# Kernel optimization log

Hardware: AMD Instinct MI355X
Metric: run time of the kernel (lower is better)

The kernel has to match this reference:

```python
import jax, jax.numpy as jnp
import numpy as np

N, T, F = 4096, 24, 16          # nodes, seq_len, in_features
H = 128                          # temporal_hidden
NH, DO = 4, 32                   # gat num_heads, gat out_features (NH*DO == H)
SEM, PH = 64, 32                 # semantic hidden, predictor hidden
SLOPE = 0.2                      # leaky_relu negative slope
ADJ_P = 0.01                     # adjacency density


def setup_inputs() -> dict:
    key = jax.random.key(0)
    ks = jax.random.split(key, 40)
    f32 = jnp.float32

    def rn(k, shape, s=0.02):
        return jax.random.normal(k, shape, f32) * s

    features = jax.random.normal(ks[0], (N, T, F), f32)
    pos_adj = (jax.random.uniform(ks[1], (N, N)) < ADJ_P).astype(f32)
    neg_adj = (jax.random.uniform(ks[2], (N, N)) < ADJ_P).astype(f32)

    inp = dict(features=features, pos_adj=pos_adj, neg_adj=neg_adj)
    # GRU (torch layout: W_ih [3H,F], W_hh [3H,H], gate order r,z,n)
    inp['gru_Wih'] = rn(ks[3], (3 * H, F), 1.0 / np.sqrt(H))
    inp['gru_Whh'] = rn(ks[4], (3 * H, H), 1.0 / np.sqrt(H))
    inp['gru_bih'] = rn(ks[5], (3 * H,), 1.0 / np.sqrt(H))
    inp['gru_bhh'] = rn(ks[6], (3 * H,), 1.0 / np.sqrt(H))
    # GAT params (linear weights stored [in, out] so we use x @ W)
    i = 7
    for pre in ('pos', 'neg'):
        inp[pre + '_W'] = rn(ks[i], (H, NH * DO)); i += 1
        inp[pre + '_u'] = rn(ks[i], (NH, DO, 1), 1.0); i += 1
        inp[pre + '_v'] = rn(ks[i], (NH, DO, 1), 1.0); i += 1
        inp[pre + '_b'] = rn(ks[i], (1, NH * DO)); i += 1
        inp[pre + '_pW'] = rn(ks[i], (H, NH * DO)); i += 1
        inp[pre + '_pb'] = jnp.zeros((NH * DO,), f32)
    inp['self_W'] = rn(ks[i], (H, H)); i += 1
    inp['self_b'] = jnp.zeros((H,), f32)
    inp['mpos_W'] = rn(ks[i], (NH * DO, H)); i += 1
    inp['mpos_b'] = jnp.zeros((H,), f32)
    inp['mneg_W'] = rn(ks[i], (NH * DO, H)); i += 1
    inp['mneg_b'] = jnp.zeros((H,), f32)
    inp['sem_W1'] = rn(ks[i], (H, SEM)); i += 1
    inp['sem_b1'] = jnp.zeros((SEM,), f32)
    inp['sem_W2'] = rn(ks[i], (SEM, 1)); i += 1
    inp['pred_W1'] = rn(ks[i], (H, PH)); i += 1
    inp['pred_b1'] = jnp.zeros((PH,), f32)
    inp['pred_W2'] = rn(ks[i], (PH, 1)); i += 1
    inp['pred_b2'] = jnp.zeros((1,), f32)
    return inp


def _gru_last(x, Wih, Whh, bih, bhh):
    # x: [N, T, F] -> last hidden state [N, H]
    gi_all = jnp.einsum('ntf,gf->tng', x, Wih) + bih  # precompute input gates [T,N,3H]
    h0 = jnp.zeros((x.shape[0], Whh.shape[1]), x.dtype)

    def step(h, gi):
        gh = h @ Whh.T + bhh
        ir, iz, in_ = jnp.split(gi, 3, axis=-1)
        hr, hz, hn = jnp.split(gh, 3, axis=-1)
        r = jax.nn.sigmoid(ir + hr)
        z = jax.nn.sigmoid(iz + hz)
        n = jnp.tanh(in_ + r * hn)
        return (1.0 - z) * n + z * h, None

    h, _ = jax.lax.scan(step, h0, gi_all)
    return h


def _gat(x, adj, W, u, v, b, pW, pb):
    sup = (x @ W).reshape(-1, NH, DO).transpose(1, 0, 2)     # [NH, N, DO]
    f1 = jnp.matmul(sup, u).reshape(NH, 1, -1)               # [NH, 1, N]
    f2 = jnp.matmul(sup, v).reshape(NH, -1, 1)               # [NH, N, 1]
    w = jax.nn.leaky_relu(f1 + f2, SLOPE)                    # [NH, N, N]
    mw = w * adj                                             # mask
    rs = mw.sum(axis=2, keepdims=True)
    rs = jnp.where(rs == 0, jnp.ones_like(rs), rs)
    attn = mw / rs
    out = jnp.matmul(attn, sup).transpose(1, 0, 2).reshape(-1, NH * DO)
    return out + b + x @ pW + pb                             # bias + residual


def _pairnorm_si(x):
    x = x - x.mean(axis=0)
    rn = jnp.sqrt(1e-6 + (x * x).sum(axis=1, keepdims=True))
    return x / rn


def reference(features, pos_adj, neg_adj,
              gru_Wih, gru_Whh, gru_bih, gru_bhh,
              pos_W, pos_u, pos_v, pos_b, pos_pW, pos_pb,
              neg_W, neg_u, neg_v, neg_b, neg_pW, neg_pb,
              self_W, self_b, mpos_W, mpos_b, mneg_W, mneg_b,
              sem_W1, sem_b1, sem_W2,
              pred_W1, pred_b1, pred_W2, pred_b2):
    support = _gru_last(features, gru_Wih, gru_Whh, gru_bih, gru_bhh)  # [N, H]
    pos_sup = _gat(support, pos_adj, pos_W, pos_u, pos_v, pos_b, pos_pW, pos_pb)
    neg_sup = _gat(support, neg_adj, neg_W, neg_u, neg_v, neg_b, neg_pW, neg_pb)
    self_e = support @ self_W + self_b
    pos_e = pos_sup @ mpos_W + mpos_b
    neg_e = neg_sup @ mneg_W + mneg_b
    emb = jnp.stack([self_e, pos_e, neg_e], axis=1)          # [N, 3, H]
    w = jnp.tanh(emb @ sem_W1 + sem_b1) @ sem_W2             # [N, 3, 1]
    beta = jax.nn.softmax(w, axis=1)
    fused = (beta * emb).sum(axis=1)                          # [N, H]
    fused = _pairnorm_si(fused)
    h = jax.nn.relu(fused @ pred_W1 + pred_b1)               # dropout is eval no-op
    out = jax.nn.sigmoid(h @ pred_W2 + pred_b2).squeeze(-1)  # [N]
    return out
```

## Files before the change

### kernel.cpp

```cpp
#include <hip/hip_runtime.h>


#define NN 4096

typedef unsigned short u16;
typedef unsigned int   u32;
typedef unsigned long long u64;
typedef __attribute__((ext_vector_type(8))) short  short8;
typedef __attribute__((ext_vector_type(4))) float  float4v;

__device__ inline float bf2f(u16 u){ return __uint_as_float(((u32)u)<<16); }
__device__ inline u16 f2bf(float f){
  u32 x = __float_as_uint(f);
  return (u16)((x + 0x7fffu + ((x>>16)&1u))>>16);
}
__device__ inline float ldm(const void* p, int i, int bf){
  return bf ? bf2f(((const u16*)p)[i]) : ((const float*)p)[i];
}
__device__ inline u16 ldm16(const void* p, int i, int bf){
  return bf ? ((const u16*)p)[i] : f2bf(((const float*)p)[i]);
}
__device__ inline float fexp(float x){
  x = fminf(fmaxf(x,-80.f),80.f);
  return __builtin_amdgcn_exp2f(x*1.4426950408889634f);
}
__device__ inline float sigm(float x){
  return __builtin_amdgcn_rcpf(1.f + fexp(-x));
}
__device__ inline float tanhf_(float x){
  float c = fminf(fmaxf(x,-15.f),15.f);
  float e = __builtin_amdgcn_exp2f(c*2.8853900817779268f);
  return (e-1.f)*__builtin_amdgcn_rcpf(e+1.f);
}
__device__ inline float4v mfma16(short8 a, short8 b, float4v c){
  return __builtin_amdgcn_mfma_f32_16x16x32_bf16(a,b,c,0,0,0);
}

__global__ __launch_bounds__(256) void k_detect(const u32* __restrict__ adj,
                                                int* __restrict__ mflag)
{
  int i = (blockIdx.x*256 + threadIdx.x)*4;
  uint4 v = *(const uint4*)(adj + i);
  u32 acc = (v.x | v.y | v.z | v.w) & 0xFFFFu;
  unsigned long long b = __ballot(acc != 0);
  if ((threadIdx.x & 63) == 0 && b) atomicOr(mflag, 1);
}

__global__ __launch_bounds__(256) void k_imp(
  const int* __restrict__ mflag,
  const void* gWih, const void* gWhh, const void* gbih, const void* gbhh,
  const void* posW, const void* posu, const void* posv, const void* posb,
  const void* pospW, const void* pospb,
  const void* negW, const void* negu, const void* negv, const void* negb,
  const void* negpW, const void* negpb,
  const void* selfW, const void* selfb, const void* mposW, const void* mposb,
  const void* mnegW, const void* mnegb,
  const void* semW1, const void* semb1, const void* semW2,
  const void* predW1, const void* predb1, const void* predW2, const void* predb2,
  u16* __restrict__ Wihb, u16* __restrict__ Whhb,
  u16* __restrict__ WT1,  u16* __restrict__ WT2,
  float* __restrict__ cbrz, float* __restrict__ cbin, float* __restrict__ cbhn,
  float* __restrict__ cuv,  float* __restrict__ cgb,  float* __restrict__ csb,
  float* __restrict__ cw1,  float* __restrict__ cb1,  float* __restrict__ cw2,
  float* __restrict__ cpw1, float* __restrict__ cpb1, float* __restrict__ cpw2,
  float* __restrict__ cpb2)
{
  const int bf = mflag[0];
  int i = blockIdx.x*256 + threadIdx.x;
  if (i < 6144){ Wihb[i]=ldm16(gWih,i,bf); return; }  i-=6144;
  if (i < 49152){ Whhb[i]=ldm16(gWhh,i,bf); return; } i-=49152;
  if (i < 81920){
    int m=i>>7,k=i&127,sel=m>>7,ml=m&127;
    const void* s = sel==0?posW: sel==1?pospW: sel==2?negW: sel==3?negpW: selfW;
    WT1[i]=ldm16(s,k*128+ml,bf); return;
  } i-=81920;
  if (i < 32768){
    int m=i>>7,k=i&127;
    const void* s = (m<128)? mposW : mnegW;
    WT2[i]=ldm16(s,k*128+(m&127),bf); return;
  } i-=32768;
  if (i < 256){ cbrz[i]=ldm(gbih,i,bf)+ldm(gbhh,i,bf); return; } i-=256;
  if (i < 128){ cbin[i]=ldm(gbih,256+i,bf); return; } i-=128;
  if (i < 128){ cbhn[i]=ldm(gbhh,256+i,bf); return; } i-=128;
  if (i < 512){
    int s=i>>8, rem=i&255, wh=rem>>7, hd=rem&127;
    const void* p = s? (wh? negv:negu) : (wh? posv:posu);
    cuv[i]=ldm(p,hd,bf); return;
  } i-=512;
  if (i < 256){
    int s=i>>7, d=i&127;
    cgb[i]=ldm(s?negb:posb,d,bf)+ldm(s?negpb:pospb,d,bf); return;
  } i-=256;
  if (i < 384){
    int t=i>>7, d=i&127;
    const void* p = t==0? selfb : t==1? mposb : mnegb;
    csb[i]=ldm(p,d,bf); return;
  } i-=384;
  if (i < 8192){ cw1[i]=ldm(semW1,i,bf); return; } i-=8192;
  if (i < 64){ cb1[i]=ldm(semb1,i,bf); return; } i-=64;
  if (i < 64){ cw2[i]=ldm(semW2,i,bf); return; } i-=64;
  if (i < 4096){ cpw1[i]=ldm(predW1,i,bf); return; } i-=4096;
  if (i < 32){ cpb1[i]=ldm(predb1,i,bf); return; } i-=32;
  if (i < 32){ cpw2[i]=ldm(predW2,i,bf); return; } i-=32;
  if (i < 1){ cpb2[i]=ldm(predb2,i,bf); return; }
}

__global__ __launch_bounds__(256) void k_csr(
  const int* __restrict__ mflag,
  const void* posadj, const void* negadj,
  int* __restrict__ deg, u16* __restrict__ idx)
{
  const int bf = mflag[0];
  const int s = blockIdx.y;
  const void* adj = s? negadj : posadj;
  const int row  = blockIdx.x*4 + (threadIdx.x>>6);
  const int lane = threadIdx.x&63;
  u16* out = idx + ((size_t)s*NN + row)*128;
  u64 mask = 0;
  if (bf){
    const uint4* rp = (const uint4*)((const u16*)adj + (size_t)row*4096);
    uint4 v[8];
    #pragma unroll
    for (int it=0; it<8; it++) v[it] = rp[it*64 + lane];
    #pragma unroll
    for (int it=0; it<8; it++){
      u32 w[4]={v[it].x,v[it].y,v[it].z,v[it].w};
      #pragma unroll
      for (int q=0;q<4;q++){
        if (w[q]&0xffffu) mask |= 1ull<<(it*8+2*q);
        if (w[q]>>16)     mask |= 1ull<<(it*8+2*q+1);
      }
    }
  } else {
    const uint4* rp = (const uint4*)((const float*)adj + (size_t)row*4096);
    uint4 v[16];
    #pragma unroll
    for (int it=0; it<16; it++) v[it] = rp[it*64 + lane];
    #pragma unroll
    for (int it=0; it<16; it++){
      if (v[it].x) mask |= 1ull<<(it*4+0);
      if (v[it].y) mask |= 1ull<<(it*4+1);
      if (v[it].z) mask |= 1ull<<(it*4+2);
      if (v[it].w) mask |= 1ull<<(it*4+3);
    }
  }
  int cnt = __popcll(mask);
  int pre = cnt;
  #pragma unroll
  for (int off=1; off<64; off<<=1){
    int o = __shfl_up(pre, off);
    if (lane>=off) pre += o;
  }
  int base = pre - cnt;
  int total = __shfl(pre, 63);
  u64 mm = mask; int k = 0;
  while (mm){
    int b = __ffsll(mm)-1; mm &= mm-1;
    int e = bf ? ((b>>3)*512 + lane*8 + (b&7))
               : ((b>>2)*256 + lane*4 + (b&3));
    int p = base + k; k++;
    if (p<128) out[p] = (u16)e;
  }
  if (lane==0) deg[s*NN+row] = total>128 ? 128 : total;
}

__global__ __launch_bounds__(512) void k_gru(
  const int* __restrict__ mflag, const void* feat,
  const u16* __restrict__ Wihb, const u16* __restrict__ Whhb,
  const float* __restrict__ cbrz, const float* __restrict__ cbin,
  const float* __restrict__ cbhn, u16* __restrict__ supb)
{
  __shared__ __attribute__((aligned(16))) u16 sh_x[16*392];
  __shared__ __attribute__((aligned(16))) u16 hbuf[2][16*136];

  const int tid=threadIdx.x, lane=tid&63, wv=tid>>6;
  const int quad=lane>>4, c15=lane&15;
  const int n0=blockIdx.x*16;
  const int bf=mflag[0];

  if (bf){
    const u16* f16p=(const u16*)feat;
    for (int i=tid;i<16*384;i+=512){ int n=i/384,e=i-n*384; sh_x[n*392+e]=f16p[(size_t)(n0+n)*384+e]; }
  } else {
    const float* f32p=(const float*)feat;
    for (int i=tid;i<16*384;i+=512){ int n=i/384,e=i-n*384; sh_x[n*392+e]=f2bf(f32p[(size_t)(n0+n)*384+e]); }
  }
  for (int i=tid;i<16*136;i+=512) hbuf[0][i]=0;

  const short8 z8={0,0,0,0,0,0,0,0};
  const float4v z4={0.f,0.f,0.f,0.f};

  short8 bh[3][4], bx[3];
  #pragma unroll
  for (int g=0;g<3;g++){
    int rowb=(g*8+wv)*16+c15;
    #pragma unroll
    for (int ks=0;ks<4;ks++) bh[g][ks]=*(const short8*)(Whhb+(size_t)rowb*128+ks*32+quad*8);
    bx[g] = (quad<2)? *(const short8*)(Wihb+(size_t)rowb*16+quad*8) : z8;
  }

  const int j0=wv*16+c15;
  const float brz_r=cbrz[j0], brz_z=cbrz[128+j0];
  const float bin0=cbin[j0],  bhn0=cbhn[j0];

  float hr[4]={0.f,0.f,0.f,0.f};

  __syncthreads();

  for (int t=0;t<24;t++){
    const u16* hb  = hbuf[t&1];
    u16*       hbn = hbuf[(t+1)&1];
    short8 ah[4];
    #pragma unroll
    for (int ks=0;ks<4;ks++) ah[ks]=*(const short8*)(hb + c15*136 + ks*32 + quad*8);
    short8 ax = (quad<2)? *(const short8*)(sh_x + c15*392 + t*16 + quad*8) : z8;

    float4v racc = mfma16(ax,bx[0],z4);
    float4v zacc = mfma16(ax,bx[1],z4);
    float4v ni   = mfma16(ax,bx[2],z4);
    float4v nh   = z4;
    #pragma unroll
    for (int ks=0;ks<4;ks++){
      racc = mfma16(ah[ks],bh[0][ks],racc);
      zacc = mfma16(ah[ks],bh[1][ks],zacc);
      nh   = mfma16(ah[ks],bh[2][ks],nh);
    }
    #pragma unroll
    for (int rr=0;rr<4;rr++){
      const int node = quad*4+rr;
      float r_ = sigm(racc[rr]+brz_r);
      float z_ = sigm(zacc[rr]+brz_z);
      float n_ = tanhf_(ni[rr]+bin0 + r_*(nh[rr]+bhn0));
      float hv = (1.f-z_)*n_ + z_*hr[rr];
      hr[rr]=hv; hbn[node*136+j0]=f2bf(hv);
    }
    __syncthreads();
  }
  #pragma unroll
  for (int rr=0;rr<4;rr++){
    const int node=quad*4+rr;
    supb[(size_t)(n0+node)*128+j0]=f2bf(hr[rr]);
  }
}

__global__ __launch_bounds__(256) void k_lin1(
  const u16* __restrict__ supb, const u16* __restrict__ WT1, float* __restrict__ C1)
{
  __shared__ __attribute__((aligned(16))) u16 sA[16*136];
  const int tid=threadIdx.x, lane=tid&63, wv=tid>>6, quad=lane>>4, c15=lane&15;
  const int n0=blockIdx.x*16;
  for (int i=tid;i<2048;i+=256){ int n=i>>7,k=i&127; sA[n*136+k]=supb[(size_t)(n0+n)*128+k]; }
  __syncthreads();
  short8 a[4];
  #pragma unroll
  for (int ks=0;ks<4;ks++) a[ks]=*(const short8*)(sA+c15*136+ks*32+quad*8);
  for (int q=0;q<10;q++){
    int tile=wv*10+q;
    float4v acc={0.f,0.f,0.f,0.f};
    #pragma unroll
    for (int ks=0;ks<4;ks++){
      short8 b=*(const short8*)(WT1+(size_t)(tile*16+c15)*128+ks*32+quad*8);
      acc=mfma16(a[ks],b,acc);
    }
    #pragma unroll
    for (int r=0;r<4;r++) C1[(size_t)(n0+quad*4+r)*640 + tile*16 + c15]=acc[r];
  }
}

__global__ __launch_bounds__(256) void k_f12(const float* __restrict__ C1,
  const float* __restrict__ cuv, float* __restrict__ f12)
{
  int id = blockIdx.x*256+threadIdx.x;
  int n=id&4095, h=(id>>12)&3, which=(id>>14)&1, s=id>>15;
  const float* uv = cuv + s*256 + which*128;
  const float* SL = C1 + (size_t)n*640 + s*256 + h*32;
  float t=0.f;
  #pragma unroll
  for (int d=0;d<32;d++) t += SL[d]*uv[h*32+d];
  f12[id]=t;
}

__global__ __launch_bounds__(256) void k_gat(
  const float* __restrict__ C1, const float* __restrict__ f12,
  const int* __restrict__ deg, const u16* __restrict__ idx,
  const float* __restrict__ cgb, u16* __restrict__ spnb)
{
  const int s=blockIdx.y;
  const int i=blockIdx.x*4 + (threadIdx.x>>6);
  const int lane=threadIdx.x&63;
  const int d0=lane, d1=lane+64, h0=d0>>5, h1=d1>>5;
  const float* f1 = f12 + s*32768;
  const float* f2 = f12 + s*32768 + 16384;
  const float f2v0=f2[h0*4096+i], f2v1=f2[h1*4096+i];
  const u16* nb = idx + ((size_t)s*NN+i)*128;
  const int dg = deg[s*NN+i];
  float acc0=0.f,acc1=0.f,rs0=0.f,rs1=0.f;
  for (int e=0;e<dg;e++){
    int j = nb[e];
    float w0 = f1[h0*4096+j]+f2v0; w0 = w0>0.f? w0 : 0.2f*w0;
    float w1 = f1[h1*4096+j]+f2v1; w1 = w1>0.f? w1 : 0.2f*w1;
    const float* SL = C1 + (size_t)j*640 + s*256;
    acc0 += w0*SL[d0]; acc1 += w1*SL[d1];
    rs0 += w0; rs1 += w1;
  }
  if (rs0==0.f) rs0=1.f;
  if (rs1==0.f) rs1=1.f;
  const float* P = C1 + (size_t)i*640 + s*256 + 128;
  float o0 = acc0/rs0 + cgb[s*128+d0] + P[d0];
  float o1 = acc1/rs1 + cgb[s*128+d1] + P[d1];
  size_t o = ((size_t)s*NN + i)*128;
  spnb[o+d0]=f2bf(o0); spnb[o+d1]=f2bf(o1);
}

__global__ __launch_bounds__(256) void k_lin2(
  const u16* __restrict__ spnb, const u16* __restrict__ WT2, float* __restrict__ E)
{
  const int s=blockIdx.y;
  __shared__ __attribute__((aligned(16))) u16 sA[16*136];
  const int tid=threadIdx.x, lane=tid&63, wv=tid>>6, quad=lane>>4, c15=lane&15;
  const int n0=blockIdx.x*16;
  const u16* A = spnb + (size_t)s*NN*128;
  for (int i=tid;i<2048;i+=256){ int n=i>>7,k=i&127; sA[n*136+k]=A[(size_t)(n0+n)*128+k]; }
  __syncthreads();
  short8 a[4];
  #pragma unroll
  for (int ks=0;ks<4;ks++) a[ks]=*(const short8*)(sA+c15*136+ks*32+quad*8);
  #pragma unroll
  for (int q=0;q<2;q++){
    int tile=wv*2+q;
    float4v acc={0.f,0.f,0.f,0.f};
    #pragma unroll
    for (int ks=0;ks<4;ks++){
      short8 b=*(const short8*)(WT2+(size_t)(s*128+tile*16+c15)*128+ks*32+quad*8);
      acc=mfma16(a[ks],b,acc);
    }
    #pragma unroll
    for (int r=0;r<4;r++) E[(size_t)(n0+quad*4+r)*256 + s*128 + tile*16 + c15]=acc[r];
  }
}

__global__ __launch_bounds__(256) void k_sem(
  const float* __restrict__ C1, const float* __restrict__ E,
  const float* __restrict__ csb, const float* __restrict__ cw1,
  const float* __restrict__ cb1, const float* __restrict__ cw2,
  float* __restrict__ fused)
{
  __shared__ float sW1[128*64];
  __shared__ float sW2[64];
  __shared__ float sb1[64];
  __shared__ float sE[4][3][128];
  const int tid=threadIdx.x, wv=tid>>6, lane=tid&63;
  for (int i=tid;i<8192;i+=256) sW1[i]=cw1[i];
  if (tid<64){ sW2[tid]=cw2[tid]; sb1[tid]=cb1[tid]; }
  const int n = blockIdx.x*4 + wv;
  for (int d=lane; d<128; d+=64){
    sE[wv][0][d] = C1[(size_t)n*640+512+d] + csb[d];
    sE[wv][1][d] = E[(size_t)n*256 + d]    + csb[128+d];
    sE[wv][2][d] = E[(size_t)n*256+128+d]  + csb[256+d];
  }
  __syncthreads();
  float sc[3];
  #pragma unroll
  for (int s=0;s<3;s++){
    float t = sb1[lane];
    for (int k=0;k<128;k++) t += sE[wv][s][k]*sW1[k*64+lane];
    t = tanhf_(t);
    float p = t*sW2[lane];
    #pragma unroll
    for (int off=32; off; off>>=1) p += __shfl_xor(p, off);
    sc[s]=p;
  }
  float mx = fmaxf(sc[0], fmaxf(sc[1],sc[2]));
  float e0=fexp(sc[0]-mx), e1=fexp(sc[1]-mx), e2=fexp(sc[2]-mx);
  float inv = 1.f/(e0+e1+e2);
  float b0=e0*inv, b1=e1*inv, b2=e2*inv;
  for (int d=lane; d<128; d+=64)
    fused[(size_t)n*128+d] = b0*sE[wv][0][d] + b1*sE[wv][1][d] + b2*sE[wv][2][d];
}

__global__ __launch_bounds__(256) void k_mean(const float* __restrict__ fused,
                                              float* __restrict__ mean)
{
  const int d = blockIdx.x;
  float s=0.f;
  for (int n=threadIdx.x; n<NN; n+=256) s += fused[(size_t)n*128+d];
  __shared__ float red[256];
  red[threadIdx.x]=s; __syncthreads();
  for (int o=128;o;o>>=1){ if (threadIdx.x<o) red[threadIdx.x]+=red[threadIdx.x+o]; __syncthreads(); }
  if (!threadIdx.x) mean[d]=red[0]*(1.f/4096.f);
}

__global__ __launch_bounds__(256) void k_pred(
  const float* __restrict__ fused, const float* __restrict__ mean,
  const float* __restrict__ cpw1, const float* __restrict__ cpb1,
  const float* __restrict__ cpw2, const float* __restrict__ cpb2,
  float* __restrict__ out)
{
  __shared__ float sy[4][128];
  __shared__ float sW1[128*32];
  __shared__ float sW2[32];
  const int tid=threadIdx.x, wv=tid>>6, lane=tid&63;
  for (int i=tid;i<4096;i+=256) sW1[i]=cpw1[i];
  if (tid<32) sW2[tid]=cpw2[tid];
  const int n = blockIdx.x*4 + wv;
  float x0 = fused[(size_t)n*128+lane]    - mean[lane];
  float x1 = fused[(size_t)n*128+64+lane] - mean[64+lane];
  float ss = x0*x0 + x1*x1;
  #pragma unroll
  for (int o=32;o;o>>=1) ss += __shfl_xor(ss,o);
  float ir = 1.f/sqrtf(1e-6f + ss);
  sy[wv][lane]=x0*ir; sy[wv][64+lane]=x1*ir;
  __syncthreads();
  float h=0.f;
  if (lane<32){
    h = cpb1[lane];
    for (int k=0;k<128;k++) h += sy[wv][k]*sW1[k*32+lane];
    h = h>0.f? h : 0.f;
    h = h*sW2[lane];
  }
  #pragma unroll
  for (int o=32;o;o>>=1) h += __shfl_xor(h,o);
  if (!lane){
    float z = h + cpb2[0];
    out[n] = __builtin_amdgcn_rcpf(1.f + fexp(-z));
  }
}

extern "C" void kernel_launch(void* const* d_in, const int* in_sizes, int n_in,
                              void* d_out, int out_size, void* d_ws, size_t ws_size,
                              hipStream_t stream)
{
  const void* feat  =d_in[0];
  const void* posadj=d_in[1];
  const void* negadj=d_in[2];
  const void* gWih  =d_in[3];
  const void* gWhh  =d_in[4];
  const void* gbih  =d_in[5];
  const void* gbhh  =d_in[6];
  const void* posW  =d_in[7];
  const void* posu  =d_in[8];
  const void* posv  =d_in[9];
  const void* posb  =d_in[10];
  const void* pospW =d_in[11];
  const void* pospb =d_in[12];
  const void* negW  =d_in[13];
  const void* negu  =d_in[14];
  const void* negv  =d_in[15];
  const void* negb  =d_in[16];
  const void* negpW =d_in[17];
  const void* negpb =d_in[18];
  const void* selfW =d_in[19];
  const void* selfb =d_in[20];
  const void* mposW =d_in[21];
  const void* mposb =d_in[22];
  const void* mnegW =d_in[23];
  const void* mnegb =d_in[24];
  const void* semW1 =d_in[25];
  const void* semb1 =d_in[26];
  const void* semW2 =d_in[27];
  const void* predW1=d_in[28];
  const void* predb1=d_in[29];
  const void* predW2=d_in[30];
  const void* predb2=d_in[31];

  char* wsb=(char*)d_ws; size_t off=0;
  auto alloc=[&](size_t bytes)->void*{ void* p=wsb+off; off+=(bytes+255)&~(size_t)255; return p; };
  int*   mflag=(int*)  alloc(256);
  u16*   Wihb =(u16*)  alloc(6144*2);
  u16*   Whhb =(u16*)  alloc(49152*2);
  u16*   WT1  =(u16*)  alloc(81920*2);
  u16*   WT2  =(u16*)  alloc(32768*2);
  float* cbrz =(float*)alloc(256*4);
  float* cbin =(float*)alloc(128*4);
  float* cbhn =(float*)alloc(128*4);
  float* cuv  =(float*)alloc(512*4);
  float* cgb  =(float*)alloc(256*4);
  float* csb  =(float*)alloc(384*4);
  float* cw1  =(float*)alloc(8192*4);
  float* cb1  =(float*)alloc(64*4);
  float* cw2  =(float*)alloc(64*4);
  float* cpw1 =(float*)alloc(4096*4);
  float* cpb1 =(float*)alloc(32*4);
  float* cpw2 =(float*)alloc(32*4);
  float* cpb2 =(float*)alloc(4);
  u16*   supb =(u16*)  alloc((size_t)NN*128*2);
  float* C1   =(float*)alloc((size_t)NN*640*4);
  float* f12  =(float*)alloc((size_t)65536*4);
  int*   deg  =(int*)  alloc((size_t)2*NN*4);
  u16*   nidx =(u16*)  alloc((size_t)2*NN*128*2);
  u16*   spnb =(u16*)  alloc((size_t)2*NN*128*2);
  float* E    =(float*)alloc((size_t)NN*256*4);
  float* fused=(float*)alloc((size_t)NN*128*4);
  float* mean =(float*)alloc(128*4);
  (void)ws_size; (void)in_sizes; (void)n_in; (void)out_size;

  hipMemsetAsync(mflag, 0, 4, stream);
  k_detect<<<16,             256,0,stream>>>((const u32*)posadj,mflag);
  k_imp   <<<720,            256,0,stream>>>(mflag,gWih,gWhh,gbih,gbhh,
              posW,posu,posv,posb,pospW,pospb,negW,negu,negv,negb,negpW,negpb,
              selfW,selfb,mposW,mposb,mnegW,mnegb,semW1,semb1,semW2,
              predW1,predb1,predW2,predb2,
              Wihb,Whhb,WT1,WT2,cbrz,cbin,cbhn,cuv,cgb,csb,cw1,cb1,cw2,
              cpw1,cpb1,cpw2,cpb2);
  k_csr <<<dim3(NN/4,2),     256,0,stream>>>(mflag,posadj,negadj,deg,nidx);
  k_gru <<<NN/16,            512,0,stream>>>(mflag,feat,Wihb,Whhb,cbrz,cbin,cbhn,supb);
  k_lin1<<<NN/16,            256,0,stream>>>(supb,WT1,C1);
  k_f12 <<<256,              256,0,stream>>>(C1,cuv,f12);
  k_gat <<<dim3(NN/4,2),     256,0,stream>>>(C1,f12,deg,nidx,cgb,spnb);
  k_lin2<<<dim3(NN/16,2),    256,0,stream>>>(spnb,WT2,E);
  k_sem <<<NN/4,             256,0,stream>>>(C1,E,csb,cw1,cb1,cw2,fused);
  k_mean<<<128,              256,0,stream>>>(fused,mean);
  k_pred<<<NN/4,             256,0,stream>>>(fused,mean,cpw1,cpb1,cpw2,cpb2,(float*)d_out);
}
```

Measured before the change: 323.2 us.

## Split CSR rows across waves, fuse f12 into lin1, stage GAT weights, atomic mean

The CSR build now uses two waves per adjacency row, each scanning half the row and claiming output slots through an atomicAdd on the degree counter. This adds parallelism to the stage that streams the adjacency matrices. The f12 attention-score kernel is folded into the tail of lin1, and the GAT kernel precomputes per-edge leaky-relu weights into shared memory so they are not recomputed inside the aggregation loop. The mean reduction becomes a column-parallel partial sum with atomics. Because the two half-rows claim slots in whatever order their atomics land, neighbour order within a row is no longer deterministic, so float summation order can vary between runs.

```diff
diff --git a/kernel.cpp b/kernel.cpp
--- a/kernel.cpp
+++ b/kernel.cpp
@@ -113,55 +113,52 @@
   const int bf = mflag[0];
   const int s = blockIdx.y;
   const void* adj = s? negadj : posadj;
-  const int row  = blockIdx.x*4 + (threadIdx.x>>6);
   const int lane = threadIdx.x&63;
-  u16* out = idx + ((size_t)s*NN + row)*128;
-  u64 mask = 0;
+  const int hr   = blockIdx.x*4 + (threadIdx.x>>6);
+  const int row  = hr>>1, half = hr&1;
+  u32 mask = 0;
   if (bf){
-    const uint4* rp = (const uint4*)((const u16*)adj + (size_t)row*4096);
-    uint4 v[8];
-    #pragma unroll
-    for (int it=0; it<8; it++) v[it] = rp[it*64 + lane];
-    #pragma unroll
-    for (int it=0; it<8; it++){
-      u32 w[4]={v[it].x,v[it].y,v[it].z,v[it].w};
-      #pragma unroll
-      for (int q=0;q<4;q++){
-        if (w[q]&0xffffu) mask |= 1ull<<(it*8+2*q);
-        if (w[q]>>16)     mask |= 1ull<<(it*8+2*q+1);
-      }
+    const u16* rp = (const u16*)adj + (size_t)row*4096 + half*2048;
+    #pragma unroll
+    for (int q=0;q<4;q++){
+      uint4 v = *(const uint4*)(rp + q*512 + lane*8);
+      if (v.x&0xffffu) mask|=1u<<(q*8+0); if (v.x>>16) mask|=1u<<(q*8+1);
+      if (v.y&0xffffu) mask|=1u<<(q*8+2); if (v.y>>16) mask|=1u<<(q*8+3);
+      if (v.z&0xffffu) mask|=1u<<(q*8+4); if (v.z>>16) mask|=1u<<(q*8+5);
+      if (v.w&0xffffu) mask|=1u<<(q*8+6); if (v.w>>16) mask|=1u<<(q*8+7);
     }
   } else {
-    const uint4* rp = (const uint4*)((const float*)adj + (size_t)row*4096);
-    uint4 v[16];
-    #pragma unroll
-    for (int it=0; it<16; it++) v[it] = rp[it*64 + lane];
-    #pragma unroll
-    for (int it=0; it<16; it++){
-      if (v[it].x) mask |= 1ull<<(it*4+0);
-      if (v[it].y) mask |= 1ull<<(it*4+1);
-      if (v[it].z) mask |= 1ull<<(it*4+2);
-      if (v[it].w) mask |= 1ull<<(it*4+3);
-    }
-  }
-  int cnt = __popcll(mask);
+    const float* rp = (const float*)adj + (size_t)row*4096 + half*2048;
+    #pragma unroll
+    for (int q=0;q<8;q++){
+      uint4 v = *(const uint4*)(rp + q*256 + lane*4);
+      if (v.x) mask|=1u<<(q*4+0);
+      if (v.y) mask|=1u<<(q*4+1);
+      if (v.z) mask|=1u<<(q*4+2);
+      if (v.w) mask|=1u<<(q*4+3);
+    }
+  }
+  int cnt = __popc(mask);
   int pre = cnt;
   #pragma unroll
   for (int off=1; off<64; off<<=1){
     int o = __shfl_up(pre, off);
     if (lane>=off) pre += o;
   }
-  int base = pre - cnt;
-  int total = __shfl(pre, 63);
-  u64 mm = mask; int k = 0;
+  int tot = __shfl(pre, 63);
+  int wbase = 0;
+  if (lane==0) wbase = atomicAdd(&deg[s*NN+row], tot);
+  wbase = __shfl(wbase, 0);
+  int base_p = wbase + pre - cnt;
+  u16* out = idx + ((size_t)s*NN + row)*128;
+  u32 mm = mask; int k = 0;
   while (mm){
-    int b = __ffsll(mm)-1; mm &= mm-1;
-    int e = bf ? ((b>>3)*512 + lane*8 + (b&7))
-               : ((b>>2)*256 + lane*4 + (b&3));
-    int p = base + k; k++;
+    int b = __ffs(mm)-1; mm &= mm-1;
+    int e = bf ? (half*2048 + (b>>3)*512 + lane*8 + (b&7))
+               : (half*2048 + (b>>2)*256 + lane*4 + (b&3));
+    int p = base_p + k; k++;
     if (p<128) out[p] = (u16)e;
   }
-  if (lane==0) deg[s*NN+row] = total>128 ? 128 : total;
 }
 
 __global__ __launch_bounds__(512) void k_gru(
@@ -244,7 +241,9 @@
 }
 
 __global__ __launch_bounds__(256) void k_lin1(
-  const u16* __restrict__ supb, const u16* __restrict__ WT1, float* __restrict__ C1)
+  const u16* __restrict__ supb, const u16* __restrict__ WT1,
+  const float* __restrict__ cuv, float* __restrict__ C1,
+  float* __restrict__ f12)
 {
   __shared__ __attribute__((aligned(16))) u16 sA[16*136];
   const int tid=threadIdx.x, lane=tid&63, wv=tid>>6, quad=lane>>4, c15=lane&15;
@@ -265,19 +264,16 @@
     #pragma unroll
     for (int r=0;r<4;r++) C1[(size_t)(n0+quad*4+r)*640 + tile*16 + c15]=acc[r];
   }
-}
-
-__global__ __launch_bounds__(256) void k_f12(const float* __restrict__ C1,
-  const float* __restrict__ cuv, float* __restrict__ f12)
-{
-  int id = blockIdx.x*256+threadIdx.x;
-  int n=id&4095, h=(id>>12)&3, which=(id>>14)&1, s=id>>15;
-  const float* uv = cuv + s*256 + which*128;
-  const float* SL = C1 + (size_t)n*640 + s*256 + h*32;
-  float t=0.f;
-  #pragma unroll
-  for (int d=0;d<32;d++) t += SL[d]*uv[h*32+d];
-  f12[id]=t;
+  __syncthreads();
+  for (int q=tid; q<512; q+=256){
+    int nl=q&15, h=(q>>4)&3, wsel=(q>>6)&1, s=(q>>7)&1;
+    const float* uvp = cuv + s*256 + wsel*128 + h*32;
+    const float* SL  = C1 + (size_t)(n0+nl)*640 + s*256 + h*32;
+    float t=0.f;
+    #pragma unroll
+    for (int d=0;d<32;d++) t += SL[d]*uvp[d];
+    f12[s*32768 + wsel*16384 + h*4096 + (n0+nl)] = t;
+  }
 }
 
 __global__ __launch_bounds__(256) void k_gat(
@@ -285,23 +281,38 @@
   const int* __restrict__ deg, const u16* __restrict__ idx,
   const float* __restrict__ cgb, u16* __restrict__ spnb)
 {
+  __shared__ u16   nbuf[4][128];
+  __shared__ float wbuf[4][4][128];
   const int s=blockIdx.y;
-  const int i=blockIdx.x*4 + (threadIdx.x>>6);
+  const int wv=threadIdx.x>>6;
+  const int i=blockIdx.x*4 + wv;
   const int lane=threadIdx.x&63;
-  const int d0=lane, d1=lane+64, h0=d0>>5, h1=d1>>5;
+  const int d0=lane, d1=lane+64, h0=lane>>5, h1=2+(lane>>5);
   const float* f1 = f12 + s*32768;
   const float* f2 = f12 + s*32768 + 16384;
-  const float f2v0=f2[h0*4096+i], f2v1=f2[h1*4096+i];
+  const int dgr = deg[s*NN+i];
+  const int dg  = dgr>128 ? 128 : dgr;
   const u16* nb = idx + ((size_t)s*NN+i)*128;
-  const int dg = deg[s*NN+i];
+  ((u32*)nbuf[wv])[lane] = ((const u32*)nb)[lane];
+  float f2v[4];
+  #pragma unroll
+  for (int h=0;h<4;h++) f2v[h]=f2[h*4096+i];
+  for (int e=lane; e<dg; e+=64){
+    int j = nbuf[wv][e];
+    #pragma unroll
+    for (int h=0;h<4;h++){
+      float w = f1[h*4096+j] + f2v[h];
+      wbuf[wv][h][e] = w>0.f ? w : 0.2f*w;
+    }
+  }
   float acc0=0.f,acc1=0.f,rs0=0.f,rs1=0.f;
   for (int e=0;e<dg;e++){
-    int j = nb[e];
-    float w0 = f1[h0*4096+j]+f2v0; w0 = w0>0.f? w0 : 0.2f*w0;
-    float w1 = f1[h1*4096+j]+f2v1; w1 = w1>0.f? w1 : 0.2f*w1;
+    float w0 = wbuf[wv][h0][e];
+    float w1 = wbuf[wv][h1][e];
+    int j = nbuf[wv][e];
     const float* SL = C1 + (size_t)j*640 + s*256;
-    acc0 += w0*SL[d0]; acc1 += w1*SL[d1];
-    rs0 += w0; rs1 += w1;
+    acc0 += w0*SL[d0]; rs0 += w0;
+    acc1 += w1*SL[d1]; rs1 += w1;
   }
   if (rs0==0.f) rs0=1.f;
   if (rs1==0.f) rs1=1.f;
@@ -379,19 +390,19 @@
 }
 
 __global__ __launch_bounds__(256) void k_mean(const float* __restrict__ fused,
-                                              float* __restrict__ mean)
-{
-  const int d = blockIdx.x;
+                                              float* __restrict__ meanacc)
+{
+  const int d = threadIdx.x & 127, h2 = threadIdx.x >> 7;
+  const int n0 = blockIdx.x*128;
   float s=0.f;
-  for (int n=threadIdx.x; n<NN; n+=256) s += fused[(size_t)n*128+d];
+  for (int n=n0+h2; n<n0+128; n+=2) s += fused[(size_t)n*128+d];
   __shared__ float red[256];
   red[threadIdx.x]=s; __syncthreads();
-  for (int o=128;o;o>>=1){ if (threadIdx.x<o) red[threadIdx.x]+=red[threadIdx.x+o]; __syncthreads(); }
-  if (!threadIdx.x) mean[d]=red[0]*(1.f/4096.f);
+  if (threadIdx.x<128) atomicAdd(&meanacc[threadIdx.x], red[threadIdx.x]+red[threadIdx.x+128]);
 }
 
 __global__ __launch_bounds__(256) void k_pred(
-  const float* __restrict__ fused, const float* __restrict__ mean,
+  const float* __restrict__ fused, const float* __restrict__ meanacc,
   const float* __restrict__ cpw1, const float* __restrict__ cpb1,
   const float* __restrict__ cpw2, const float* __restrict__ cpb2,
   float* __restrict__ out)
@@ -403,8 +414,9 @@
   for (int i=tid;i<4096;i+=256) sW1[i]=cpw1[i];
   if (tid<32) sW2[tid]=cpw2[tid];
   const int n = blockIdx.x*4 + wv;
-  float x0 = fused[(size_t)n*128+lane]    - mean[lane];
-  float x1 = fused[(size_t)n*128+64+lane] - mean[64+lane];
+  const float inv_n = 1.f/4096.f;
+  float x0 = fused[(size_t)n*128+lane]    - meanacc[lane]*inv_n;
+  float x1 = fused[(size_t)n*128+64+lane] - meanacc[64+lane]*inv_n;
   float ss = x0*x0 + x1*x1;
   #pragma unroll
   for (int o=32;o;o>>=1) ss += __shfl_xor(ss,o);
@@ -491,10 +503,12 @@
   u16*   spnb =(u16*)  alloc((size_t)2*NN*128*2);
   float* E    =(float*)alloc((size_t)NN*256*4);
   float* fused=(float*)alloc((size_t)NN*128*4);
-  float* mean =(float*)alloc(128*4);
+  float* meanacc=(float*)alloc(128*4);
   (void)ws_size; (void)in_sizes; (void)n_in; (void)out_size;
 
   hipMemsetAsync(mflag, 0, 4, stream);
+  hipMemsetAsync(deg, 0, (size_t)2*NN*4, stream);
+  hipMemsetAsync(meanacc, 0, 128*4, stream);
   k_detect<<<16,             256,0,stream>>>((const u32*)posadj,mflag);
   k_imp   <<<720,            256,0,stream>>>(mflag,gWih,gWhh,gbih,gbhh,
               posW,posu,posv,posb,pospW,pospb,negW,negu,negv,negb,negpW,negpb,
@@ -502,13 +516,12 @@
               predW1,predb1,predW2,predb2,
               Wihb,Whhb,WT1,WT2,cbrz,cbin,cbhn,cuv,cgb,csb,cw1,cb1,cw2,
               cpw1,cpb1,cpw2,cpb2);
-  k_csr <<<dim3(NN/4,2),     256,0,stream>>>(mflag,posadj,negadj,deg,nidx);
+  k_csr <<<dim3(2048,2),     256,0,stream>>>(mflag,posadj,negadj,deg,nidx);
   k_gru <<<NN/16,            512,0,stream>>>(mflag,feat,Wihb,Whhb,cbrz,cbin,cbhn,supb);
-  k_lin1<<<NN/16,            256,0,stream>>>(supb,WT1,C1);
-  k_f12 <<<256,              256,0,stream>>>(C1,cuv,f12);
+  k_lin1<<<NN/16,            256,0,stream>>>(supb,WT1,cuv,C1,f12);
   k_gat <<<dim3(NN/4,2),     256,0,stream>>>(C1,f12,deg,nidx,cgb,spnb);
   k_lin2<<<dim3(NN/16,2),    256,0,stream>>>(spnb,WT2,E);
   k_sem <<<NN/4,             256,0,stream>>>(C1,E,csb,cw1,cb1,cw2,fused);
-  k_mean<<<128,              256,0,stream>>>(fused,mean);
-  k_pred<<<NN/4,             256,0,stream>>>(fused,mean,cpw1,cpb1,cpw2,cpb2,(float*)d_out);
-}
+  k_mean<<<32,               256,0,stream>>>(fused,meanacc);
+  k_pred<<<NN/4,             256,0,stream>>>(fused,meanacc,cpw1,cpb1,cpw2,cpb2,(float*)d_out);
+}
```

Result: no change. 321.3 us (-0.6%).
